# Kernel optimization log

Measured on AMD Instinct MI355X. Metric: run time of the kernel, lower is better.

The kernel has to match this reference:

```python
import jax, jax.numpy as jnp
import numpy as np

C = 16  # number of classes (matches batch_ids fill_max)
XMIN, XMAX = 1e-37, 1.0 - 1e-5

def setup_inputs() -> dict:
    key = jax.random.key(0)
    k1, k2 = jax.random.split(key)
    hidden = jax.random.normal(k1, (65536, 512), dtype=jnp.float32)
    batch_ids = jax.random.randint(k2, (65536,), 0, C, dtype=jnp.int64)
    return {"hidden": hidden, "batch_ids": batch_ids, "d": 64}

def reference(hidden, batch_ids, d):
    N, D = hidden.shape
    seg = lambda v: jax.ops.segment_sum(v, batch_ids, num_segments=C)
    counts = seg(jnp.ones((N,), hidden.dtype))                  # [C]
    means = seg(hidden) / counts[:, None]                       # [C, D]
    # within-class sum of squared deviations, per feature dim
    withins = seg((hidden - means[batch_ids]) ** 2)             # [C, D]
    # pairwise: global mean of pair is (m_i+m_j)/2, so each class's between
    # term is ((m_i-m_j)/2)^2; weighted by counts it sums to that * (n_i+n_j)
    half_diff = (means[:, None, :] - means[None, :, :]) * 0.5   # [C, C, D]
    pair_counts = counts[:, None] + counts[None, :]             # [C, C]
    pair_between = half_diff * half_diff * pair_counts[:, :, None]
    pair_within = withins[:, None, :] + withins[None, :, :]
    d2 = pair_counts - 2.0
    d2 = jnp.where(d2 == 0.0, 1e-5, d2)
    x = pair_between / (pair_between + pair_within)
    x = jnp.clip(x, XMIN, XMAX)
    a = jnp.full_like(x, 0.5)                                   # d1/2
    b = jnp.broadcast_to((d2 * 0.5)[:, :, None], x.shape)       # d2/2
    xbetainc = jax.scipy.special.betainc(a, b, x)               # [C, C, D]
    top_k, _ = jax.lax.top_k(xbetainc, d)                       # [C, C, d]
    per_pair = jnp.sum(jnp.log(top_k), axis=-1)                 # [C, C]
    mask = jnp.triu(jnp.ones((C, C), dtype=bool), k=1)          # pairs i<j
    total = jnp.sum(jnp.where(mask, per_pair, jnp.zeros_like(per_pair)))
    return -total
```

## Files before the change

kernel.cpp:

```cpp
#include <hip/hip_runtime.h>
#include <math.h>

#define NUM_C 16
#define DIMS 512
#define RPC 128
#define NCHUNK 512
#define GRP 16
#define CPG (NCHUNK / GRP)

__device__ inline void atomAddF(float* p, float v) { unsafeAtomicAdd(p, v); }


__global__ __launch_bounds__(256) void k_stream(const float* __restrict__ hidden,
                                                const int* __restrict__ bids,
                                                float* __restrict__ psum,
                                                float* __restrict__ psq,
                                                int* __restrict__ pcnt) {
    __shared__ float lsum[NUM_C * 256];
    __shared__ float lsq[NUM_C * 256];
    const int tid = threadIdx.x;
    const int g = blockIdx.x & 1;
    const int chunk = blockIdx.x >> 1;

    #pragma unroll
    for (int c = 0; c < NUM_C; ++c) { lsum[c * 256 + tid] = 0.f; lsq[c * 256 + tid] = 0.f; }

    const int rowbase = chunk * RPC;
    const float* hp = hidden + (size_t)rowbase * DIMS + g * 256 + tid;
    const int* bp = bids + rowbase;

    int mycnt = 0;

    float va[8]; int ca[8];
    #pragma unroll
    for (int u = 0; u < 8; ++u) { va[u] = hp[(size_t)u * DIMS]; ca[u] = bp[u]; }

    for (int it = 0; it < RPC / 8 - 1; ++it) {
        float vb[8]; int cb[8];
        const float* hp2 = hp + (size_t)(it + 1) * 8 * DIMS;
        const int* bp2 = bp + (it + 1) * 8;
        #pragma unroll
        for (int u = 0; u < 8; ++u) { vb[u] = hp2[(size_t)u * DIMS]; cb[u] = bp2[u]; }
        #pragma unroll
        for (int u = 0; u < 8; ++u) {
            const int idx = ca[u] * 256 + tid;
            lsum[idx] += va[u];
            lsq[idx]  += va[u] * va[u];
            mycnt += (ca[u] == tid) ? 1 : 0;
        }
        #pragma unroll
        for (int u = 0; u < 8; ++u) { va[u] = vb[u]; ca[u] = cb[u]; }
    }
    #pragma unroll
    for (int u = 0; u < 8; ++u) {
        const int idx = ca[u] * 256 + tid;
        lsum[idx] += va[u];
        lsq[idx]  += va[u] * va[u];
        mycnt += (ca[u] == tid) ? 1 : 0;
    }

    float* ps = psum + (size_t)blockIdx.x * NUM_C * 256 + tid;
    float* pq = psq  + (size_t)blockIdx.x * NUM_C * 256 + tid;
    #pragma unroll
    for (int c = 0; c < NUM_C; ++c) {
        ps[c * 256] = lsum[c * 256 + tid];
        pq[c * 256] = lsq[c * 256 + tid];
    }
    if (g == 0 && tid < NUM_C) pcnt[chunk * NUM_C + tid] = mycnt;
}

__global__ __launch_bounds__(256) void k_reduce(const float* __restrict__ psum,
                                                const float* __restrict__ psq,
                                                const int* __restrict__ pcnt,
                                                float* __restrict__ p2sum,
                                                float* __restrict__ p2sq,
                                                int* __restrict__ cnt2,
                                                float* __restrict__ out) {
    const int tid = threadIdx.x;
    const int bid = blockIdx.x;
    const int c = bid >> 5;
    const int g = (bid >> 4) & 1;
    const int grp = bid & 15;
    if (bid == 0 && tid == 0) out[0] = 0.f;

    float s = 0.f, q = 0.f;
    #pragma unroll 4
    for (int k = 0; k < CPG; ++k) {
        const int chunk = grp * CPG + k;
        const size_t seg = ((size_t)(chunk * 2 + g) * NUM_C + c) * 256 + tid;
        s += psum[seg];
        q += psq[seg];
    }
    p2sum[((c * 2 + g) * GRP + grp) * 256 + tid] = s;
    p2sq [((c * 2 + g) * GRP + grp) * 256 + tid] = q;

    if (g == 0 && tid == 0) {
        int cc = 0;
        for (int k = 0; k < CPG; ++k) cc += pcnt[(grp * CPG + k) * NUM_C + c];
        cnt2[c * GRP + grp] = cc;
    }
}

__global__ __launch_bounds__(512) void k_pairs(const float* __restrict__ p2sum,
                                               const float* __restrict__ p2sq,
                                               const int* __restrict__ cnt2,
                                               const int* __restrict__ dptr,
                                               float* __restrict__ out) {
    __shared__ float xs[DIMS];
    __shared__ float wsum[8];
    const int tid = threadIdx.x;

    int p = blockIdx.x, i = 0, rem = p;
    while (rem >= NUM_C - 1 - i) { rem -= NUM_C - 1 - i; ++i; }
    const int j = i + 1 + rem;

    int cnti = 0, cntj = 0;
    #pragma unroll
    for (int gq = 0; gq < GRP; ++gq) { cnti += cnt2[i * GRP + gq]; cntj += cnt2[j * GRP + gq]; }
    const float ni = (float)cnti, nj = (float)cntj;
    const float pc = ni + nj;

    {
        const int g = tid >> 8, dl = tid & 255;
        float si = 0.f, qi = 0.f, sj = 0.f, qj = 0.f;
        #pragma unroll
        for (int gq = 0; gq < GRP; ++gq) {
            si += p2sum[((i * 2 + g) * GRP + gq) * 256 + dl];
            qi += p2sq [((i * 2 + g) * GRP + gq) * 256 + dl];
            sj += p2sum[((j * 2 + g) * GRP + gq) * 256 + dl];
            qj += p2sq [((j * 2 + g) * GRP + gq) * 256 + dl];
        }
        const float mi = si / ni, mj = sj / nj;
        float wi = qi - si * mi;  wi = wi > 0.f ? wi : 0.f;
        float wj = qj - sj * mj;  wj = wj > 0.f ? wj : 0.f;
        const float hd = (mi - mj) * 0.5f;
        const float between = hd * hd * pc;
        const float within = wi + wj;
        float x = between / (between + within);
        if (!(x >= 1e-37f)) x = 1e-37f;
        const float XM = 1.0f - 1e-5f;
        if (x > XM) x = XM;
        xs[tid] = x;
    }

    for (int kk = 2; kk <= DIMS; kk <<= 1) {
        for (int jj = kk >> 1; jj > 0; jj >>= 1) {
            __syncthreads();
            const int ixj = tid ^ jj;
            if (ixj > tid) {
                const float va = xs[tid], vb = xs[ixj];
                const bool sw = ((tid & kk) == 0) ? (va < vb) : (va > vb);
                if (sw) { xs[tid] = vb; xs[ixj] = va; }
            }
        }
    }
    __syncthreads();

    const int d = *dptr;
    float d2 = pc - 2.0f;
    if (d2 == 0.0f) d2 = 1e-5f;
    const float b = d2 * 0.5f;
    const float bm1 = b - 1.0f;
    const float invb = 1.0f / b;
    const float ln2overB = 0.69314718f
        - (0.5f * (1.14472989f - logf(b)) + log1pf(invb * (0.125f + 0.0078125f * invb)));

    const int sub = tid & 7;
    const int rounds = (d + 63) >> 6;
    float part = 0.f;
    for (int r = 0; r < rounds; ++r) {
        const int q = (tid >> 3) + (r << 6);
        const bool act = (q < d);
        const float x = xs[act ? q : 0];
        const float rt = sqrtf(x);
        const float h = rt * (1.0f / 256.0f);
        float acc = 0.f;
        for (int k = sub; k <= 256; k += 8) {
            const float sv = (float)k * h;
            const float w = (k == 0 || k == 256) ? 1.f : ((k & 1) ? 4.f : 2.f);
            acc += w * __expf(bm1 * log1pf(-sv * sv));
        }
        acc += __shfl_down(acc, 4, 64);
        acc += __shfl_down(acc, 2, 64);
        acc += __shfl_down(acc, 1, 64);
        if (sub == 0 && act) {
            float li = logf(acc * h * (1.0f / 3.0f)) + ln2overB;
            part += (li < 0.f) ? li : 0.f;
        }
    }
    for (int off = 32; off > 0; off >>= 1) part += __shfl_down(part, off, 64);
    if ((tid & 63) == 0) wsum[tid >> 6] = part;
    __syncthreads();
    if (tid == 0) {
        float t = 0.f;
        for (int w = 0; w < 8; ++w) t += wsum[w];
        atomAddF(out, -t);
    }
}

extern "C" void kernel_launch(void* const* d_in, const int* in_sizes, int n_in,
                              void* d_out, int out_size, void* d_ws, size_t ws_size,
                              hipStream_t stream) {
    const float* hidden = (const float*)d_in[0];
    const int* bids = (const int*)d_in[1];
    const int* dptr = (const int*)d_in[2];
    float* out = (float*)d_out;

    char* ws = (char*)d_ws;
    float* psum  = (float*)(ws);
    float* psq   = (float*)(ws + (16u << 20));
    int*   pcnt  = (int*)  (ws + (32u << 20));
    float* p2sum = (float*)(ws + (32u << 20) + 32768);
    float* p2sq  = (float*)(ws + (32u << 20) + 32768 + 524288);
    int*   cnt2  = (int*)  (ws + (32u << 20) + 32768 + 2 * 524288);

    k_stream<<<NCHUNK * 2, 256, 0, stream>>>(hidden, bids, psum, psq, pcnt);
    k_reduce<<<NUM_C * 2 * GRP, 256, 0, stream>>>(psum, psq, pcnt, p2sum, p2sq, cnt2, out);
    k_pairs <<<NUM_C * (NUM_C - 1) / 2, 512, 0, stream>>>(p2sum, p2sq, cnt2, dptr, out);
}
```

Baseline: 227.6 us.

## Interleave sum and sum-of-squares as float2 and double rows per chunk

Stores the per-class sum and sum-of-squares accumulators interleaved as float2 in shared memory and in the workspace, so each update and each partial read or write moves both values in one access. The rows handled per streaming block double while the chunk count halves, which halves the partial-sum traffic written to and read back from global memory. The cost is fewer streaming blocks, 512 instead of 1024, which lowers parallelism for the main pass over hidden. The float2 shared-memory accesses may also change LDS bank behaviour.

```diff
diff --git a/kernel.cpp b/kernel.cpp
--- a/kernel.cpp
+++ b/kernel.cpp
@@ -3,8 +3,8 @@
 
 #define NUM_C 16
 #define DIMS 512
-#define RPC 128
-#define NCHUNK 512
+#define RPC 256
+#define NCHUNK 256
 #define GRP 16
 #define CPG (NCHUNK / GRP)
 
@@ -13,17 +13,15 @@
 
 __global__ __launch_bounds__(256) void k_stream(const float* __restrict__ hidden,
                                                 const int* __restrict__ bids,
-                                                float* __restrict__ psum,
-                                                float* __restrict__ psq,
+                                                float2* __restrict__ psum,
                                                 int* __restrict__ pcnt) {
-    __shared__ float lsum[NUM_C * 256];
-    __shared__ float lsq[NUM_C * 256];
+    __shared__ float2 acc[NUM_C * 256];
     const int tid = threadIdx.x;
     const int g = blockIdx.x & 1;
     const int chunk = blockIdx.x >> 1;
 
     #pragma unroll
-    for (int c = 0; c < NUM_C; ++c) { lsum[c * 256 + tid] = 0.f; lsq[c * 256 + tid] = 0.f; }
+    for (int c = 0; c < NUM_C; ++c) acc[c * 256 + tid] = make_float2(0.f, 0.f);
 
     const int rowbase = chunk * RPC;
     const float* hp = hidden + (size_t)rowbase * DIMS + g * 256 + tid;
@@ -44,8 +42,10 @@
         #pragma unroll
         for (int u = 0; u < 8; ++u) {
             const int idx = ca[u] * 256 + tid;
-            lsum[idx] += va[u];
-            lsq[idx]  += va[u] * va[u];
+            float2 a = acc[idx];
+            a.x += va[u];
+            a.y += va[u] * va[u];
+            acc[idx] = a;
             mycnt += (ca[u] == tid) ? 1 : 0;
         }
         #pragma unroll
@@ -54,26 +54,22 @@
     #pragma unroll
     for (int u = 0; u < 8; ++u) {
         const int idx = ca[u] * 256 + tid;
-        lsum[idx] += va[u];
-        lsq[idx]  += va[u] * va[u];
+        float2 a = acc[idx];
+        a.x += va[u];
+        a.y += va[u] * va[u];
+        acc[idx] = a;
         mycnt += (ca[u] == tid) ? 1 : 0;
     }
 
-    float* ps = psum + (size_t)blockIdx.x * NUM_C * 256 + tid;
-    float* pq = psq  + (size_t)blockIdx.x * NUM_C * 256 + tid;
-    #pragma unroll
-    for (int c = 0; c < NUM_C; ++c) {
-        ps[c * 256] = lsum[c * 256 + tid];
-        pq[c * 256] = lsq[c * 256 + tid];
-    }
+    float2* ps = psum + (size_t)blockIdx.x * NUM_C * 256 + tid;
+    #pragma unroll
+    for (int c = 0; c < NUM_C; ++c) ps[c * 256] = acc[c * 256 + tid];
     if (g == 0 && tid < NUM_C) pcnt[chunk * NUM_C + tid] = mycnt;
 }
 
-__global__ __launch_bounds__(256) void k_reduce(const float* __restrict__ psum,
-                                                const float* __restrict__ psq,
+__global__ __launch_bounds__(256) void k_reduce(const float2* __restrict__ psum,
                                                 const int* __restrict__ pcnt,
-                                                float* __restrict__ p2sum,
-                                                float* __restrict__ p2sq,
+                                                float2* __restrict__ p2,
                                                 int* __restrict__ cnt2,
                                                 float* __restrict__ out) {
     const int tid = threadIdx.x;
@@ -87,22 +83,20 @@
     #pragma unroll 4
     for (int k = 0; k < CPG; ++k) {
         const int chunk = grp * CPG + k;
-        const size_t seg = ((size_t)(chunk * 2 + g) * NUM_C + c) * 256 + tid;
-        s += psum[seg];
-        q += psq[seg];
-    }
-    p2sum[((c * 2 + g) * GRP + grp) * 256 + tid] = s;
-    p2sq [((c * 2 + g) * GRP + grp) * 256 + tid] = q;
+        const float2 v = psum[((size_t)(chunk * 2 + g) * NUM_C + c) * 256 + tid];
+        s += v.x; q += v.y;
+    }
+    p2[((c * 2 + g) * GRP + grp) * 256 + tid] = make_float2(s, q);
 
     if (g == 0 && tid == 0) {
         int cc = 0;
+        #pragma unroll
         for (int k = 0; k < CPG; ++k) cc += pcnt[(grp * CPG + k) * NUM_C + c];
         cnt2[c * GRP + grp] = cc;
     }
 }
 
-__global__ __launch_bounds__(512) void k_pairs(const float* __restrict__ p2sum,
-                                               const float* __restrict__ p2sq,
+__global__ __launch_bounds__(512) void k_pairs(const float2* __restrict__ p2,
                                                const int* __restrict__ cnt2,
                                                const int* __restrict__ dptr,
                                                float* __restrict__ out) {
@@ -125,10 +119,10 @@
         float si = 0.f, qi = 0.f, sj = 0.f, qj = 0.f;
         #pragma unroll
         for (int gq = 0; gq < GRP; ++gq) {
-            si += p2sum[((i * 2 + g) * GRP + gq) * 256 + dl];
-            qi += p2sq [((i * 2 + g) * GRP + gq) * 256 + dl];
-            sj += p2sum[((j * 2 + g) * GRP + gq) * 256 + dl];
-            qj += p2sq [((j * 2 + g) * GRP + gq) * 256 + dl];
+            const float2 a = p2[((i * 2 + g) * GRP + gq) * 256 + dl];
+            const float2 b = p2[((j * 2 + g) * GRP + gq) * 256 + dl];
+            si += a.x; qi += a.y;
+            sj += b.x; qj += b.y;
         }
         const float mi = si / ni, mj = sj / nj;
         float wi = qi - si * mi;  wi = wi > 0.f ? wi : 0.f;
@@ -207,14 +201,12 @@
     float* out = (float*)d_out;
 
     char* ws = (char*)d_ws;
-    float* psum  = (float*)(ws);
-    float* psq   = (float*)(ws + (16u << 20));
-    int*   pcnt  = (int*)  (ws + (32u << 20));
-    float* p2sum = (float*)(ws + (32u << 20) + 32768);
-    float* p2sq  = (float*)(ws + (32u << 20) + 32768 + 524288);
-    int*   cnt2  = (int*)  (ws + (32u << 20) + 32768 + 2 * 524288);
-
-    k_stream<<<NCHUNK * 2, 256, 0, stream>>>(hidden, bids, psum, psq, pcnt);
-    k_reduce<<<NUM_C * 2 * GRP, 256, 0, stream>>>(psum, psq, pcnt, p2sum, p2sq, cnt2, out);
-    k_pairs <<<NUM_C * (NUM_C - 1) / 2, 512, 0, stream>>>(p2sum, p2sq, cnt2, dptr, out);
-}
+    float2* psum = (float2*)(ws);
+    int*    pcnt = (int*)   (ws + (16u << 20));
+    float2* p2   = (float2*)(ws + (16u << 20) + 16384);
+    int*    cnt2 = (int*)   (ws + (16u << 20) + 16384 + (1u << 20));
+
+    k_stream<<<NCHUNK * 2, 256, 0, stream>>>(hidden, bids, psum, pcnt);
+    k_reduce<<<NUM_C * 2 * GRP, 256, 0, stream>>>(psum, pcnt, p2, cnt2, out);
+    k_pairs <<<NUM_C * (NUM_C - 1) / 2, 512, 0, stream>>>(p2, cnt2, dptr, out);
+}
```

New measurement: 224.4 us. No clear change (-1.4%).
